# Kernel tuning notes

Measured on AMD Instinct MI355X. Metric: run time of the kernel, lower is better.

The kernel has to match this reference:

```python
import jax, jax.numpy as jnp
import numpy as np

B, S, E, H = 4, 1024, 512, 8
DK = E // H


def setup_inputs() -> dict:
    key = jax.random.key(0)
    ks = jax.random.split(key, 16)
    s = 1.0 / np.sqrt(E)
    inp = {
        "query": jax.random.normal(ks[0], (B, S, E), dtype=jnp.float32),
        "key": jax.random.normal(ks[1], (B, S, E), dtype=jnp.float32),
        "value": jax.random.normal(ks[2], (B, S, E), dtype=jnp.float32),
        "dist_conv": jax.random.uniform(ks[3], (B, S, S), dtype=jnp.float32),
        "mask": jax.random.randint(ks[4], (B, S, S), 0, 2, dtype=jnp.int32),
        # four Linear(E, E) layers: q, k, v, out (torch: y = x @ W.T + b)
        "Wq": jax.random.normal(ks[5], (E, E), dtype=jnp.float32) * s,
        "bq": jnp.zeros((E,), dtype=jnp.float32),
        "Wk": jax.random.normal(ks[6], (E, E), dtype=jnp.float32) * s,
        "bk": jnp.zeros((E,), dtype=jnp.float32),
        "Wv": jax.random.normal(ks[7], (E, E), dtype=jnp.float32) * s,
        "bv": jnp.zeros((E,), dtype=jnp.float32),
        "Wo": jax.random.normal(ks[8], (E, E), dtype=jnp.float32) * s,
        "bo": jnp.zeros((E,), dtype=jnp.float32),
        # 1x1 Conv2d(1, H) -> ReLU -> 1x1 Conv2d(H, H)
        "cw1": jax.random.normal(ks[9], (H,), dtype=jnp.float32),  # [out_c] (in_c=1, k=1)
        "cb1": jnp.zeros((H,), dtype=jnp.float32),
        "cw2": jax.random.normal(ks[10], (H, H), dtype=jnp.float32) * (1.0 / np.sqrt(H)),
        "cb2": jnp.zeros((H,), dtype=jnp.float32),
    }
    return inp


def reference(query, key, value, dist_conv, mask, Wq, bq, Wk, bk, Wv, bv, Wo, bo, cw1, cb1, cw2, cb2):
    # projections, split into heads: [B, H, S, DK]
    def proj(x, W, b):
        y = jnp.einsum("bse,fe->bsf", x, W) + b
        return y.reshape(B, S, H, DK).transpose(0, 2, 1, 3)

    q = proj(query, Wq, bq)
    k = proj(key, Wk, bk)
    v = proj(value, Wv, bv)

    # 1x1 conv stack on distance matrix: [B,S,S] -> [B,H,S,S]
    t = jax.nn.relu(dist_conv[:, None] * cw1[None, :, None, None] + cb1[None, :, None, None])
    bias = jnp.einsum("bhij,gh->bgij", t, cw2) + cb2[None, :, None, None]

    scores = jnp.einsum("bhqd,bhkd->bhqk", q, k) / jnp.sqrt(jnp.float32(DK))
    scores = scores * bias
    scores = jnp.where(mask[:, None] == 0, jnp.float32(-1e9), scores)
    p_attn = jax.nn.softmax(scores, axis=-1)

    x = jnp.einsum("bhqk,bhkd->bhqd", p_attn, v)
    x = x.transpose(0, 2, 1, 3).reshape(B, S, E)
    return jnp.einsum("bse,fe->bsf", x, Wo) + bo
```

## Files before the change

### kernel.cpp

```cpp
#include <hip/hip_runtime.h>
#include <hip/hip_bf16.h>
#include <math.h>

#define B_ 4
#define S_ 1024
#define E_ 512
#define H_ 8
#define DK_ 64

typedef short bf16x8 __attribute__((ext_vector_type(8)));
typedef float f32x4 __attribute__((ext_vector_type(4)));

#define MFMA16(a, b, c) __builtin_amdgcn_mfma_f32_16x16x32_bf16((a), (b), (c), 0, 0, 0)

__device__ __forceinline__ void gl_lds16(const void* gptr, void* lptr) {
    __builtin_amdgcn_global_load_lds(
        (const __attribute__((address_space(1))) unsigned int*)gptr,
        (__attribute__((address_space(3))) unsigned int*)lptr,
        16, 0, 0);
}

__global__ __launch_bounds__(256) void convert_bf16(
    const float* __restrict__ q, const float* __restrict__ k, const float* __restrict__ v,
    const float* __restrict__ wq, const float* __restrict__ wk,
    const float* __restrict__ wv, const float* __restrict__ wo,
    const float* __restrict__ dist, const int* __restrict__ mask,
    __hip_bfloat16* qc, __hip_bfloat16* kc, __hip_bfloat16* vc,
    __hip_bfloat16* wqc, __hip_bfloat16* wkc, __hip_bfloat16* wvc, __hip_bfloat16* woc,
    float* md) {
    const int z = blockIdx.y;
    const int idx = (blockIdx.x * 256 + threadIdx.x) * 8;
    if (z == 7) {
        if (idx >= B_ * S_ * S_) return;
        float4 d0 = *(const float4*)(dist + idx);
        float4 d1 = *(const float4*)(dist + idx + 4);
        int4 m0 = *(const int4*)(mask + idx);
        int4 m1 = *(const int4*)(mask + idx + 4);
        float4 o0, o1;
        o0.x = m0.x ? d0.x : -1.0f; o0.y = m0.y ? d0.y : -1.0f;
        o0.z = m0.z ? d0.z : -1.0f; o0.w = m0.w ? d0.w : -1.0f;
        o1.x = m1.x ? d1.x : -1.0f; o1.y = m1.y ? d1.y : -1.0f;
        o1.z = m1.z ? d1.z : -1.0f; o1.w = m1.w ? d1.w : -1.0f;
        *(float4*)(md + idx) = o0;
        *(float4*)(md + idx + 4) = o1;
        return;
    }
    const float* src;
    __hip_bfloat16* dst;
    int n;
    switch (z) {
        case 0: src = q;  dst = qc;  n = B_ * S_ * E_; break;
        case 1: src = k;  dst = kc;  n = B_ * S_ * E_; break;
        case 2: src = v;  dst = vc;  n = B_ * S_ * E_; break;
        case 3: src = wq; dst = wqc; n = E_ * E_; break;
        case 4: src = wk; dst = wkc; n = E_ * E_; break;
        case 5: src = wv; dst = wvc; n = E_ * E_; break;
        default: src = wo; dst = woc; n = E_ * E_; break;
    }
    if (idx >= n) return;
    float4 a = *(const float4*)(src + idx);
    float4 bb = *(const float4*)(src + idx + 4);
    union { __hip_bfloat16 h[8]; uint4 u; } o;
    o.h[0] = __float2bfloat16(a.x);  o.h[1] = __float2bfloat16(a.y);
    o.h[2] = __float2bfloat16(a.z);  o.h[3] = __float2bfloat16(a.w);
    o.h[4] = __float2bfloat16(bb.x); o.h[5] = __float2bfloat16(bb.y);
    o.h[6] = __float2bfloat16(bb.z); o.h[7] = __float2bfloat16(bb.w);
    *(uint4*)(dst + idx) = o.u;
}

__device__ __forceinline__ void gemm_core(const __hip_bfloat16* A, const __hip_bfloat16* W,
                                          char* sA, char* sW, int m0, int n0,
                                          f32x4 acc[4][2]) {
    const int t = threadIdx.x;
    const int w = t >> 6, lane = t & 63;
    const int wm = (w >> 1) * 64, wn = (w & 1) * 32;
    const int g = lane >> 4, ln = lane & 15;

    for (int kc = 0; kc < 8; ++kc) {
        __syncthreads();
#pragma unroll
        for (int i = 0; i < 4; ++i) {
            int L = (i * 4 + w) * 64 + lane;
            int r = L >> 3, cs = L & 7;
            int c = cs ^ (r & 7);
            gl_lds16((const char*)A + (size_t)(m0 + r) * 1024 + kc * 128 + c * 16,
                     sA + (i * 4 + w) * 1024);
        }
#pragma unroll
        for (int i = 0; i < 2; ++i) {
            int L = (i * 4 + w) * 64 + lane;
            int r = L >> 3, cs = L & 7;
            int c = cs ^ (r & 7);
            gl_lds16((const char*)W + (size_t)(n0 + r) * 1024 + kc * 128 + c * 16,
                     sW + (i * 4 + w) * 1024);
        }
        __syncthreads();
#pragma unroll
        for (int ks = 0; ks < 2; ++ks) {
            bf16x8 af[4], bf[2];
#pragma unroll
            for (int mt = 0; mt < 4; ++mt) {
                int m = wm + mt * 16 + ln;
                int c = ks * 4 + g;
                af[mt] = *(const bf16x8*)(sA + m * 128 + (c ^ (m & 7)) * 16);
            }
#pragma unroll
            for (int nt = 0; nt < 2; ++nt) {
                int n = wn + nt * 16 + ln;
                int c = ks * 4 + g;
                bf[nt] = *(const bf16x8*)(sW + n * 128 + (c ^ (n & 7)) * 16);
            }
#pragma unroll
            for (int mt = 0; mt < 4; ++mt)
#pragma unroll
                for (int nt = 0; nt < 2; ++nt)
                    acc[mt][nt] = MFMA16(af[mt], bf[nt], acc[mt][nt]);
        }
    }
}

__global__ __launch_bounds__(256) void proj_gemm(
    const __hip_bfloat16* __restrict__ qc, const __hip_bfloat16* __restrict__ kc,
    const __hip_bfloat16* __restrict__ vc,
    const __hip_bfloat16* __restrict__ wqc, const __hip_bfloat16* __restrict__ wkc,
    const __hip_bfloat16* __restrict__ wvc,
    const float* __restrict__ bq, const float* __restrict__ bk, const float* __restrict__ bv,
    __hip_bfloat16* qbh, __hip_bfloat16* kbh, __hip_bfloat16* vt) {
    __shared__ char smem[24576];
    char* sA = smem;
    char* sW = smem + 16384;
    const int z = blockIdx.z;
    const __hip_bfloat16* A;
    const __hip_bfloat16* W;
    const float* bias;
    __hip_bfloat16* dst;
    if (z == 0)      { A = qc; W = wqc; bias = bq; dst = qbh; }
    else if (z == 1) { A = kc; W = wkc; bias = bk; dst = kbh; }
    else             { A = vc; W = wvc; bias = bv; dst = vt; }

    const int m0 = blockIdx.y * 128, n0 = blockIdx.x * 64;
    f32x4 acc[4][2] = {};
    gemm_core(A, W, sA, sW, m0, n0, acc);
    __syncthreads();

    const int t = threadIdx.x;
    const int w = t >> 6, lane = t & 63;
    const int wm = (w >> 1) * 64, wn = (w & 1) * 32;
    const int g = lane >> 4, ln = lane & 15;
    const int b = m0 >> 10;
    const int hh = n0 >> 6;
    float bv2[2];
#pragma unroll
    for (int nt = 0; nt < 2; ++nt) bv2[nt] = bias[n0 + wn + nt * 16 + ln];

    __hip_bfloat16* T = (__hip_bfloat16*)smem;
    if (z != 2) {
#pragma unroll
        for (int mt = 0; mt < 4; ++mt)
#pragma unroll
            for (int nt = 0; nt < 2; ++nt)
#pragma unroll
                for (int r = 0; r < 4; ++r) {
                    int lm = wm + mt * 16 + g * 4 + r;
                    int n = wn + nt * 16 + ln;
                    T[lm * 72 + n] = __float2bfloat16(acc[mt][nt][r] + bv2[nt]);
                }
        __syncthreads();
        const int lm = t >> 1, half = t & 1;
        const char* srow = smem + lm * 144 + half * 64;
        char* gdst = (char*)dst +
                     (((size_t)(b * 8 + hh) * 1024 + (m0 & 1023) + lm) * 64) * 2 + half * 64;
#pragma unroll
        for (int j = 0; j < 4; ++j)
            *(uint4*)(gdst + j * 16) = *(const uint4*)(srow + j * 16);
    } else {
#pragma unroll
        for (int mt = 0; mt < 4; ++mt)
#pragma unroll
            for (int nt = 0; nt < 2; ++nt)
#pragma unroll
                for (int r = 0; r < 4; ++r) {
                    int lm = wm + mt * 16 + g * 4 + r;
                    int n = wn + nt * 16 + ln;
                    T[lm * 66 + n] = __float2bfloat16(acc[mt][nt][r] + bv2[nt]);
                }
        __syncthreads();
        const int dk = t >> 2, a = t & 3;
        union { __hip_bfloat16 h[32]; uint4 u[4]; } P;
#pragma unroll
        for (int i = 0; i < 32; ++i)
            P.h[i] = T[(a * 32 + i) * 66 + dk];
        char* gdst = (char*)vt +
                     (((size_t)(b * 8 + hh) * 64 + dk) * 1024 + (m0 & 1023) + a * 32) * 2;
#pragma unroll
        for (int j = 0; j < 4; ++j)
            *(uint4*)(gdst + j * 16) = P.u[j];
    }
}

__global__ __launch_bounds__(256) void out_gemm(
    const __hip_bfloat16* __restrict__ X, const __hip_bfloat16* __restrict__ woc,
    const float* __restrict__ bo, float* __restrict__ out) {
    __shared__ char smem[24576];
    char* sA = smem;
    char* sW = smem + 16384;
    const int m0 = blockIdx.y * 128, n0 = blockIdx.x * 64;
    f32x4 acc[4][2] = {};
    gemm_core(X, woc, sA, sW, m0, n0, acc);

    const int t = threadIdx.x;
    const int w = t >> 6, lane = t & 63;
    const int wm = (w >> 1) * 64, wn = (w & 1) * 32;
    const int g = lane >> 4, ln = lane & 15;
    float bv2[2];
#pragma unroll
    for (int nt = 0; nt < 2; ++nt) bv2[nt] = bo[n0 + wn + nt * 16 + ln];
#pragma unroll
    for (int mt = 0; mt < 4; ++mt)
#pragma unroll
        for (int nt = 0; nt < 2; ++nt)
#pragma unroll
            for (int r = 0; r < 4; ++r) {
                int m = m0 + wm + mt * 16 + g * 4 + r;
                int f = n0 + wn + nt * 16 + ln;
                out[(size_t)m * 512 + f] = acc[mt][nt][r] + bv2[nt];
            }
}

__global__ __launch_bounds__(256) void attn(
    const __hip_bfloat16* __restrict__ Qb, const __hip_bfloat16* __restrict__ Kb,
    const __hip_bfloat16* __restrict__ Vt, const float* __restrict__ md,
    const float* __restrict__ cw1, const float* __restrict__ cb1,
    const float* __restrict__ cw2, const float* __restrict__ cb2,
    __hip_bfloat16* __restrict__ X) {
    __shared__ char sK[8192];
    __shared__ char sV[8192];
    __shared__ float sSc[4][16][66];
    __shared__ __hip_bfloat16 sP[4][16][72];
    __shared__ float sBr[4][16];

    const int t = threadIdx.x, w = t >> 6, lane = t & 63;
    const int g = lane >> 4, ln = lane & 15;
    const int qr = lane >> 2, a = lane & 3;
    const int bh = blockIdx.y, b = bh >> 3, h = bh & 7;
    const int q0 = blockIdx.x * 64;

    float w1[8], b1[8], w2[8];
#pragma unroll
    for (int i = 0; i < 8; ++i) {
        w1[i] = cw1[i]; b1[i] = cb1[i]; w2[i] = cw2[h * 8 + i];
    }
    const float b2v = cb2[h];

    bf16x8 qf[2];
    {
        const char* qbase = (const char*)Qb + ((size_t)bh * 1024 + q0 + w * 16 + ln) * 128;
        qf[0] = *(const bf16x8*)(qbase + g * 16);
        qf[1] = *(const bf16x8*)(qbase + 64 + g * 16);
    }

    float m_st = -1e30f, l_st = 0.f;
    f32x4 O[4] = {};

    const size_t kbase = (size_t)bh * 1024 * 128;
    const size_t vbase = (size_t)bh * 64 * 2048;
    const float* mdrow = md + ((size_t)b * 1024 + q0 + w * 16 + qr) * 1024;

    for (int kt = 0; kt < S_; kt += 64) {
        __syncthreads();
#pragma unroll
        for (int i = 0; i < 2; ++i) {
            int L = (i * 4 + w) * 64 + lane;
            int r = L >> 3, cs = L & 7;
            int c = cs ^ (r & 7);
            gl_lds16((const char*)Kb + kbase + (size_t)(kt + r) * 128 + c * 16,
                     sK + (i * 4 + w) * 1024);
            gl_lds16((const char*)Vt + vbase + (size_t)r * 2048 + (size_t)kt * 2 + c * 16,
                     sV + (i * 4 + w) * 1024);
        }
        float4 md4[4];
#pragma unroll
        for (int j = 0; j < 4; ++j)
            md4[j] = *(const float4*)(mdrow + kt + a * 16 + j * 4);
        __syncthreads();

        f32x4 sc[4] = {};
#pragma unroll
        for (int tt = 0; tt < 4; ++tt)
#pragma unroll
            for (int ks = 0; ks < 2; ++ks) {
                int key = tt * 16 + ln;
                int c = ks * 4 + g;
                bf16x8 kf = *(const bf16x8*)(sK + key * 128 + (c ^ (key & 7)) * 16);
                sc[tt] = MFMA16(qf[ks], kf, sc[tt]);
            }

#pragma unroll
        for (int tt = 0; tt < 4; ++tt)
#pragma unroll
            for (int r = 0; r < 4; ++r)
                sSc[w][g * 4 + r][tt * 16 + ln] = sc[tt][r];

        float sr[16];
        {
            const float* scrow = &sSc[w][qr][a * 16];
#pragma unroll
            for (int j = 0; j < 8; ++j) {
                float2 v2 = *(const float2*)(scrow + j * 2);
                sr[j * 2] = v2.x; sr[j * 2 + 1] = v2.y;
            }
        }
        float mx = -1e30f;
#pragma unroll
        for (int j = 0; j < 4; ++j) {
            float dvv[4] = {md4[j].x, md4[j].y, md4[j].z, md4[j].w};
#pragma unroll
            for (int e = 0; e < 4; ++e) {
                float d = dvv[e];
                float bias_v = b2v;
#pragma unroll
                for (int hh = 0; hh < 8; ++hh) {
                    float tv = fmaf(d, w1[hh], b1[hh]);
                    tv = fmaxf(tv, 0.f);
                    bias_v = fmaf(tv, w2[hh], bias_v);
                }
                float sval = sr[j * 4 + e] * 0.125f * bias_v;
                if (d < 0.f) sval = -1e9f;
                sr[j * 4 + e] = sval;
                mx = fmaxf(mx, sval);
            }
        }
        mx = fmaxf(mx, __shfl_xor(mx, 1));
        mx = fmaxf(mx, __shfl_xor(mx, 2));
        const float mnew = fmaxf(m_st, mx);
        const float alpha = __expf(m_st - mnew);
        m_st = mnew;
        float rs = 0.f;
        union { __hip_bfloat16 hh16[16]; uint4 u[2]; } Pk;
#pragma unroll
        for (int i = 0; i < 16; ++i) {
            float p = __expf(sr[i] - mnew);
            rs += p;
            Pk.hh16[i] = __float2bfloat16(p);
        }
        rs += __shfl_xor(rs, 1);
        rs += __shfl_xor(rs, 2);
        l_st = l_st * alpha + rs;
        *(uint4*)(&sP[w][qr][a * 16]) = Pk.u[0];
        *(uint4*)(&sP[w][qr][a * 16 + 8]) = Pk.u[1];
        if (a == 0) sBr[w][qr] = alpha;
        float al4[4];
#pragma unroll
        for (int r = 0; r < 4; ++r) al4[r] = sBr[w][g * 4 + r];
#pragma unroll
        for (int tt = 0; tt < 4; ++tt)
#pragma unroll
            for (int r = 0; r < 4; ++r) O[tt][r] *= al4[r];

#pragma unroll
        for (int ks = 0; ks < 2; ++ks) {
            bf16x8 pf = *(const bf16x8*)(&sP[w][ln][ks * 32 + g * 8]);
#pragma unroll
            for (int tt = 0; tt < 4; ++tt) {
                int dk = tt * 16 + ln;
                int c = ks * 4 + g;
                bf16x8 vf = *(const bf16x8*)(sV + dk * 128 + (c ^ (dk & 7)) * 16);
                O[tt] = MFMA16(pf, vf, O[tt]);
            }
        }
    }

    if (a == 0) sBr[w][qr] = l_st;
    __builtin_amdgcn_s_waitcnt(0);
#pragma unroll
    for (int r = 0; r < 4; ++r) {
        float inv = 1.f / sBr[w][g * 4 + r];
        int q = q0 + w * 16 + g * 4 + r;
#pragma unroll
        for (int tt = 0; tt < 4; ++tt) {
            int dk = tt * 16 + ln;
            X[((size_t)(b * 1024 + q)) * 512 + h * 64 + dk] = __float2bfloat16(O[tt][r] * inv);
        }
    }
}

extern "C" void kernel_launch(void* const* d_in, const int* in_sizes, int n_in,
                              void* d_out, int out_size, void* d_ws, size_t ws_size,
                              hipStream_t stream) {
    (void)in_sizes; (void)n_in; (void)out_size; (void)ws_size;
    const float* query = (const float*)d_in[0];
    const float* key   = (const float*)d_in[1];
    const float* value = (const float*)d_in[2];
    const float* dist  = (const float*)d_in[3];
    const int*   mask  = (const int*)d_in[4];
    const float* Wq = (const float*)d_in[5];
    const float* bq = (const float*)d_in[6];
    const float* Wk = (const float*)d_in[7];
    const float* bk = (const float*)d_in[8];
    const float* Wv = (const float*)d_in[9];
    const float* bv = (const float*)d_in[10];
    const float* Wo = (const float*)d_in[11];
    const float* bo = (const float*)d_in[12];
    const float* cw1 = (const float*)d_in[13];
    const float* cb1 = (const float*)d_in[14];
    const float* cw2 = (const float*)d_in[15];
    const float* cb2 = (const float*)d_in[16];
    float* out = (float*)d_out;

    char* ws = (char*)d_ws;
    const size_t MB = 1 << 20;
    __hip_bfloat16* qc  = (__hip_bfloat16*)(ws + 0 * MB);
    __hip_bfloat16* kc  = (__hip_bfloat16*)(ws + 4 * MB);
    __hip_bfloat16* vc  = (__hip_bfloat16*)(ws + 8 * MB);
    __hip_bfloat16* wqc = (__hip_bfloat16*)(ws + 12 * MB);
    __hip_bfloat16* wkc = (__hip_bfloat16*)(ws + 12 * MB + 512 * 1024);
    __hip_bfloat16* wvc = (__hip_bfloat16*)(ws + 13 * MB);
    __hip_bfloat16* woc = (__hip_bfloat16*)(ws + 13 * MB + 512 * 1024);
    __hip_bfloat16* qbh = (__hip_bfloat16*)(ws + 14 * MB);
    __hip_bfloat16* kbh = (__hip_bfloat16*)(ws + 18 * MB);
    __hip_bfloat16* vt  = (__hip_bfloat16*)(ws + 22 * MB);
    __hip_bfloat16* x   = (__hip_bfloat16*)(ws + 26 * MB);
    float*          mdp = (float*)(ws + 30 * MB);

    hipLaunchKernelGGL(convert_bf16, dim3(2048, 8), dim3(256), 0, stream,
                       query, key, value, Wq, Wk, Wv, Wo, dist, mask,
                       qc, kc, vc, wqc, wkc, wvc, woc, mdp);
    hipLaunchKernelGGL(proj_gemm, dim3(8, 32, 3), dim3(256), 0, stream,
                       qc, kc, vc, wqc, wkc, wvc, bq, bk, bv, qbh, kbh, vt);
    hipLaunchKernelGGL(attn, dim3(16, 32), dim3(256), 0, stream,
                       qbh, kbh, vt, mdp, cw1, cb1, cw2, cb2, x);
    hipLaunchKernelGGL(out_gemm, dim3(8, 32), dim3(256), 0, stream,
                       x, woc, bo, out);
}
```

Measured before the change: 204.3 us.

## Precompute per-head conv bias in bf16 with scale and mask folded in

Adds a bias_pre kernel that computes the 1x1-conv bias for every head once, folds in the 1/sqrt(dk) scale, encodes masked entries as a bf16 sentinel, and writes a [B,H,S,S] bf16 tensor. The attention kernel then reads 16 bf16 bias values per thread instead of recomputing the 8x8 conv MLP per score from an fp32 masked-distance buffer. It also shrinks the convert grid so no blocks are idle and overlays the score and P scratch buffers in LDS. In exchange, the intermediate tensor grows to 64MB of bf16 writes plus reads, where the old masked-distance buffer was 16MB fp32, and the bias loses precision from bf16 rounding.

```diff
diff --git a/kernel.cpp b/kernel.cpp
--- a/kernel.cpp
+++ b/kernel.cpp
@@ -12,6 +12,7 @@
 typedef float f32x4 __attribute__((ext_vector_type(4)));
 
 #define MFMA16(a, b, c) __builtin_amdgcn_mfma_f32_16x16x32_bf16((a), (b), (c), 0, 0, 0)
+#define cfence() asm volatile("" ::: "memory")
 
 __device__ __forceinline__ void gl_lds16(const void* gptr, void* lptr) {
     __builtin_amdgcn_global_load_lds(
@@ -20,44 +21,35 @@
         16, 0, 0);
 }
 
+__device__ __forceinline__ unsigned short bf16_bits(float v) {
+    __hip_bfloat16 h = __float2bfloat16(v);
+    return *(unsigned short*)&h;
+}
+
 __global__ __launch_bounds__(256) void convert_bf16(
     const float* __restrict__ q, const float* __restrict__ k, const float* __restrict__ v,
     const float* __restrict__ wq, const float* __restrict__ wk,
     const float* __restrict__ wv, const float* __restrict__ wo,
-    const float* __restrict__ dist, const int* __restrict__ mask,
     __hip_bfloat16* qc, __hip_bfloat16* kc, __hip_bfloat16* vc,
-    __hip_bfloat16* wqc, __hip_bfloat16* wkc, __hip_bfloat16* wvc, __hip_bfloat16* woc,
-    float* md) {
-    const int z = blockIdx.y;
-    const int idx = (blockIdx.x * 256 + threadIdx.x) * 8;
-    if (z == 7) {
-        if (idx >= B_ * S_ * S_) return;
-        float4 d0 = *(const float4*)(dist + idx);
-        float4 d1 = *(const float4*)(dist + idx + 4);
-        int4 m0 = *(const int4*)(mask + idx);
-        int4 m1 = *(const int4*)(mask + idx + 4);
-        float4 o0, o1;
-        o0.x = m0.x ? d0.x : -1.0f; o0.y = m0.y ? d0.y : -1.0f;
-        o0.z = m0.z ? d0.z : -1.0f; o0.w = m0.w ? d0.w : -1.0f;
-        o1.x = m1.x ? d1.x : -1.0f; o1.y = m1.y ? d1.y : -1.0f;
-        o1.z = m1.z ? d1.z : -1.0f; o1.w = m1.w ? d1.w : -1.0f;
-        *(float4*)(md + idx) = o0;
-        *(float4*)(md + idx + 4) = o1;
-        return;
-    }
+    __hip_bfloat16* wqc, __hip_bfloat16* wkc, __hip_bfloat16* wvc, __hip_bfloat16* woc) {
+    const int blk = blockIdx.x;
     const float* src;
     __hip_bfloat16* dst;
-    int n;
-    switch (z) {
-        case 0: src = q;  dst = qc;  n = B_ * S_ * E_; break;
-        case 1: src = k;  dst = kc;  n = B_ * S_ * E_; break;
-        case 2: src = v;  dst = vc;  n = B_ * S_ * E_; break;
-        case 3: src = wq; dst = wqc; n = E_ * E_; break;
-        case 4: src = wk; dst = wkc; n = E_ * E_; break;
-        case 5: src = wv; dst = wvc; n = E_ * E_; break;
-        default: src = wo; dst = woc; n = E_ * E_; break;
-    }
-    if (idx >= n) return;
+    int base;
+    if (blk < 1024)      { src = q; dst = qc; base = blk; }
+    else if (blk < 2048) { src = k; dst = kc; base = blk - 1024; }
+    else if (blk < 3072) { src = v; dst = vc; base = blk - 2048; }
+    else {
+        const int wz = (blk - 3072) >> 7;
+        base = (blk - 3072) & 127;
+        switch (wz) {
+            case 0: src = wq; dst = wqc; break;
+            case 1: src = wk; dst = wkc; break;
+            case 2: src = wv; dst = wvc; break;
+            default: src = wo; dst = woc; break;
+        }
+    }
+    const int idx = (base * 256 + threadIdx.x) * 8;
     float4 a = *(const float4*)(src + idx);
     float4 bb = *(const float4*)(src + idx + 4);
     union { __hip_bfloat16 h[8]; uint4 u; } o;
@@ -66,6 +58,42 @@
     o.h[4] = __float2bfloat16(bb.x); o.h[5] = __float2bfloat16(bb.y);
     o.h[6] = __float2bfloat16(bb.z); o.h[7] = __float2bfloat16(bb.w);
     *(uint4*)(dst + idx) = o.u;
+}
+
+__global__ __launch_bounds__(256) void bias_pre(
+    const float* __restrict__ dist, const int* __restrict__ mask,
+    const float* __restrict__ cw1, const float* __restrict__ cb1,
+    const float* __restrict__ cw2, const float* __restrict__ cb2,
+    __hip_bfloat16* __restrict__ biasS) {
+    const int bi = blockIdx.x;
+    const int b = bi >> 10, i = bi & 1023;
+    const int j0 = threadIdx.x * 4;
+    const size_t dbase = ((size_t)b * 1024 + i) * 1024 + j0;
+    float4 d4 = *(const float4*)(dist + dbase);
+    int4 m4 = *(const int4*)(mask + dbase);
+    float dv[4] = {d4.x, d4.y, d4.z, d4.w};
+    int mv[4] = {m4.x, m4.y, m4.z, m4.w};
+    float tt[4][8];
+#pragma unroll
+    for (int e = 0; e < 4; ++e)
+#pragma unroll
+        for (int h = 0; h < 8; ++h)
+            tt[e][h] = fmaxf(fmaf(dv[e], cw1[h], cb1[h]), 0.f);
+#pragma unroll
+    for (int g = 0; g < 8; ++g) {
+        const float c2 = cb2[g];
+        union { unsigned short us[4]; uint2 u2; } o;
+#pragma unroll
+        for (int e = 0; e < 4; ++e) {
+            float bv = c2;
+#pragma unroll
+            for (int h = 0; h < 8; ++h) bv = fmaf(tt[e][h], cw2[g * 8 + h], bv);
+            unsigned short u = bf16_bits(bv * 0.125f);
+            if (mv[e] == 0) u = 0xFF80u;
+            o.us[e] = u;
+        }
+        *(uint2*)(biasS + ((size_t)(b * 8 + g) * 1024 + i) * 1024 + j0) = o.u2;
+    }
 }
 
 __device__ __forceinline__ void gemm_core(const __hip_bfloat16* A, const __hip_bfloat16* W,
@@ -229,28 +257,21 @@
 
 __global__ __launch_bounds__(256) void attn(
     const __hip_bfloat16* __restrict__ Qb, const __hip_bfloat16* __restrict__ Kb,
-    const __hip_bfloat16* __restrict__ Vt, const float* __restrict__ md,
-    const float* __restrict__ cw1, const float* __restrict__ cb1,
-    const float* __restrict__ cw2, const float* __restrict__ cb2,
+    const __hip_bfloat16* __restrict__ Vt, const __hip_bfloat16* __restrict__ biasS,
     __hip_bfloat16* __restrict__ X) {
     __shared__ char sK[8192];
     __shared__ char sV[8192];
-    __shared__ float sSc[4][16][66];
-    __shared__ __hip_bfloat16 sP[4][16][72];
+    __shared__ char sScP[4][4352];
     __shared__ float sBr[4][16];
 
     const int t = threadIdx.x, w = t >> 6, lane = t & 63;
     const int g = lane >> 4, ln = lane & 15;
     const int qr = lane >> 2, a = lane & 3;
-    const int bh = blockIdx.y, b = bh >> 3, h = bh & 7;
+    const int bh = blockIdx.y;
     const int q0 = blockIdx.x * 64;
 
-    float w1[8], b1[8], w2[8];
-#pragma unroll
-    for (int i = 0; i < 8; ++i) {
-        w1[i] = cw1[i]; b1[i] = cb1[i]; w2[i] = cw2[h * 8 + i];
-    }
-    const float b2v = cb2[h];
+    float* sc = (float*)(sScP[w]);
+    __hip_bfloat16* sp = (__hip_bfloat16*)(sScP[w]);
 
     bf16x8 qf[2];
     {
@@ -264,7 +285,7 @@
 
     const size_t kbase = (size_t)bh * 1024 * 128;
     const size_t vbase = (size_t)bh * 64 * 2048;
-    const float* mdrow = md + ((size_t)b * 1024 + q0 + w * 16 + qr) * 1024;
+    const __hip_bfloat16* brow = biasS + ((size_t)bh * 1024 + q0 + w * 16 + qr) * 1024;
 
     for (int kt = 0; kt < S_; kt += 64) {
         __syncthreads();
@@ -278,13 +299,12 @@
             gl_lds16((const char*)Vt + vbase + (size_t)r * 2048 + (size_t)kt * 2 + c * 16,
                      sV + (i * 4 + w) * 1024);
         }
-        float4 md4[4];
-#pragma unroll
-        for (int j = 0; j < 4; ++j)
-            md4[j] = *(const float4*)(mdrow + kt + a * 16 + j * 4);
-        __syncthreads();
-
-        f32x4 sc[4] = {};
+        union { uint4 u[2]; unsigned short us[16]; } bb;
+        bb.u[0] = *(const uint4*)(brow + kt + a * 16);
+        bb.u[1] = *(const uint4*)(brow + kt + a * 16 + 8);
+        __syncthreads();
+
+        f32x4 scv[4] = {};
 #pragma unroll
         for (int tt = 0; tt < 4; ++tt)
 #pragma unroll
@@ -292,43 +312,37 @@
                 int key = tt * 16 + ln;
                 int c = ks * 4 + g;
                 bf16x8 kf = *(const bf16x8*)(sK + key * 128 + (c ^ (key & 7)) * 16);
-                sc[tt] = MFMA16(qf[ks], kf, sc[tt]);
-            }
-
+                scv[tt] = MFMA16(qf[ks], kf, scv[tt]);
+            }
+
+        cfence();
 #pragma unroll
         for (int tt = 0; tt < 4; ++tt)
 #pragma unroll
             for (int r = 0; r < 4; ++r)
-                sSc[w][g * 4 + r][tt * 16 + ln] = sc[tt][r];
+                sc[(g * 4 + r) * 66 + tt * 16 + ln] = scv[tt][r];
+        cfence();
 
         float sr[16];
         {
-            const float* scrow = &sSc[w][qr][a * 16];
+            const float* scrow = sc + qr * 66 + a * 16;
 #pragma unroll
             for (int j = 0; j < 8; ++j) {
                 float2 v2 = *(const float2*)(scrow + j * 2);
                 sr[j * 2] = v2.x; sr[j * 2 + 1] = v2.y;
             }
         }
+        cfence();
+
         float mx = -1e30f;
 #pragma unroll
-        for (int j = 0; j < 4; ++j) {
-            float dvv[4] = {md4[j].x, md4[j].y, md4[j].z, md4[j].w};
-#pragma unroll
-            for (int e = 0; e < 4; ++e) {
-                float d = dvv[e];
-                float bias_v = b2v;
-#pragma unroll
-                for (int hh = 0; hh < 8; ++hh) {
-                    float tv = fmaf(d, w1[hh], b1[hh]);
-                    tv = fmaxf(tv, 0.f);
-                    bias_v = fmaf(tv, w2[hh], bias_v);
-                }
-                float sval = sr[j * 4 + e] * 0.125f * bias_v;
-                if (d < 0.f) sval = -1e9f;
-                sr[j * 4 + e] = sval;
-                mx = fmaxf(mx, sval);
-            }
+        for (int e = 0; e < 16; ++e) {
+            unsigned int bits = bb.us[e];
+            float f = __uint_as_float(bits << 16);
+            float s = sr[e] * f;
+            s = (bits == 0xFF80u) ? -1e9f : s;
+            sr[e] = s;
+            mx = fmaxf(mx, s);
         }
         mx = fmaxf(mx, __shfl_xor(mx, 1));
         mx = fmaxf(mx, __shfl_xor(mx, 2));
@@ -346,8 +360,11 @@
         rs += __shfl_xor(rs, 1);
         rs += __shfl_xor(rs, 2);
         l_st = l_st * alpha + rs;
-        *(uint4*)(&sP[w][qr][a * 16]) = Pk.u[0];
-        *(uint4*)(&sP[w][qr][a * 16 + 8]) = Pk.u[1];
+
+        *(uint4*)(sp + qr * 72 + a * 16) = Pk.u[0];
+        *(uint4*)(sp + qr * 72 + a * 16 + 8) = Pk.u[1];
+        cfence();
+
         if (a == 0) sBr[w][qr] = alpha;
         float al4[4];
 #pragma unroll
@@ -359,7 +376,7 @@
 
 #pragma unroll
         for (int ks = 0; ks < 2; ++ks) {
-            bf16x8 pf = *(const bf16x8*)(&sP[w][ln][ks * 32 + g * 8]);
+            bf16x8 pf = *(const bf16x8*)(sp + ln * 72 + ks * 32 + g * 8);
 #pragma unroll
             for (int tt = 0; tt < 4; ++tt) {
                 int dk = tt * 16 + ln;
@@ -368,10 +385,12 @@
                 O[tt] = MFMA16(pf, vf, O[tt]);
             }
         }
+        cfence();
     }
 
     if (a == 0) sBr[w][qr] = l_st;
     __builtin_amdgcn_s_waitcnt(0);
+    const int b = bh >> 3, h = bh & 7;
 #pragma unroll
     for (int r = 0; r < 4; ++r) {
         float inv = 1.f / sBr[w][g * 4 + r];
@@ -420,15 +439,17 @@
     __hip_bfloat16* kbh = (__hip_bfloat16*)(ws + 18 * MB);
     __hip_bfloat16* vt  = (__hip_bfloat16*)(ws + 22 * MB);
     __hip_bfloat16* x   = (__hip_bfloat16*)(ws + 26 * MB);
-    float*          mdp = (float*)(ws + 30 * MB);
-
-    hipLaunchKernelGGL(convert_bf16, dim3(2048, 8), dim3(256), 0, stream,
-                       query, key, value, Wq, Wk, Wv, Wo, dist, mask,
-                       qc, kc, vc, wqc, wkc, wvc, woc, mdp);
+    __hip_bfloat16* bS  = (__hip_bfloat16*)(ws + 32 * MB);
+
+    hipLaunchKernelGGL(convert_bf16, dim3(3584), dim3(256), 0, stream,
+                       query, key, value, Wq, Wk, Wv, Wo,
+                       qc, kc, vc, wqc, wkc, wvc, woc);
+    hipLaunchKernelGGL(bias_pre, dim3(4096), dim3(256), 0, stream,
+                       dist, mask, cw1, cb1, cw2, cb2, bS);
     hipLaunchKernelGGL(proj_gemm, dim3(8, 32, 3), dim3(256), 0, stream,
                        qc, kc, vc, wqc, wkc, wvc, bq, bk, bv, qbh, kbh, vt);
     hipLaunchKernelGGL(attn, dim3(16, 32), dim3(256), 0, stream,
-                       qbh, kbh, vt, mdp, cw1, cb1, cw2, cb2, x);
+                       qbh, kbh, vt, bS, x);
     hipLaunchKernelGGL(out_gemm, dim3(8, 32), dim3(256), 0, stream,
                        x, woc, bo, out);
 }
```

Result: no change. 200.7 us (-1.7%).
